# Kernel optimization log

Hardware: AMD Instinct MI355X
Metric: run time of the kernel (lower is better)

Reference implementation:

```python
import jax, jax.numpy as jnp
import numpy as np

B, P, D, VP, VD = 256, 1152, 10, 8, 16
NUM_ITER = 3


def setup_inputs() -> dict:
    key = jax.random.key(0)
    k1, k2 = jax.random.split(key)
    x = jax.random.normal(k1, (B, P, VP, 1), dtype=jnp.float32)
    # learned transform matrices, init randn/100 as in the torch module
    W = jax.random.normal(k2, (P, D, VD, VP), dtype=jnp.float32) / 100.0
    return {"x": x, "W": W}


def _squash(s, axis):
    # v = ||s||^2/(1+||s||^2) * s/||s||
    sq = jnp.sum(s * s, axis=axis, keepdims=True)
    return s * sq / (1.0 + sq) / jnp.sqrt(sq + 1e-9)


def reference(x, W):
    xs = x[..., 0]                                      # [B,P,8]
    # u_hat[b,p,d,:] = W[p,d] @ x[b,p]  (no explicit stack/broadcast materialization)
    u_hat = jnp.einsum('pdij,bpj->bpdi', W, xs)          # [B,P,D,16]
    u_stop = jax.lax.stop_gradient(u_hat)
    b_ij = jnp.zeros((B, P, D, 1), dtype=u_hat.dtype)    # torch b_ij [B,P,D,1,1], trailing 1 dropped
    v = None
    for it in range(NUM_ITER):
        # faithful to source: softmax over torch dim=3 (size-1 axis) -> all ones
        c_ij = jax.nn.softmax(b_ij, axis=3)               # [B,P,D,1]
        u = u_hat if it == NUM_ITER - 1 else u_stop
        s_j = jnp.sum(c_ij * u, axis=1)                   # [B,D,16]
        v = _squash(s_j, axis=2)                          # [B,D,16]
        if it != NUM_ITER - 1:
            # agreement: u_hat^T v -> scalar per (b,p,d)
            upd = jnp.einsum('bpdi,bdi->bpd', u_hat, v)[..., None]
            b_ij = b_ij + upd
    return v[..., None]                                   # [B,D,16,1] matching torch output
```

## Files before the change

### kernel.cpp

```cpp
#include <hip/hip_runtime.h>
#include <hip/hip_bf16.h>
#include <math.h>

#define M 256
#define N 160
#define K 9216
#define CH 32
#define KC 288
#define BM 32
#define XST 104

using f32x4 = __attribute__((ext_vector_type(4))) float;
using bf16x8 = __attribute__((ext_vector_type(8))) short;

__device__ __forceinline__ ushort f2bf(float f) {
  return __builtin_bit_cast(ushort, __float2bfloat16(f));
}

template <bool ATOMIC>
__global__ __launch_bounds__(256) void gemm_mfma(const float* __restrict__ x,
                                                 const float* __restrict__ W,
                                                 float* __restrict__ part) {
  __shared__ ushort Wl[12 * 1280];
  __shared__ ushort Xl[BM * XST];

  const int t = threadIdx.x;
  const int bx = blockIdx.x;
  const int mt = bx & 7;
  const int c = bx >> 3;
  const int m0 = mt * BM;
  const int k0 = c * KC;

  const int w = t >> 6;
  const int l = t & 63;
  const int lr = l & 15;
  const int lg = l >> 4;
  const int msub = w & 1;
  const int nh = w >> 1;

  float4 wv[15], xv[3];
  int xrow[3], xkq[3];
#pragma unroll
  for (int q = 0; q < 3; ++q) {
    const int f = t + 256 * q;
    xrow[q] = f / 24;
    xkq[q] = (f - xrow[q] * 24) * 4;
  }

  auto load = [&](int s) {
    const float* wsp = W + ((size_t)c * 36 + s * 12) * 1280;
#pragma unroll
    for (int q = 0; q < 15; ++q)
      wv[q] = *(const float4*)(wsp + 4 * (size_t)(t + 256 * q));
    const float* xs = x + (size_t)m0 * K + k0 + s * 96;
#pragma unroll
    for (int q = 0; q < 3; ++q)
      xv[q] = *(const float4*)(xs + (size_t)xrow[q] * K + xkq[q]);
  };
  auto put = [&]() {
#pragma unroll
    for (int q = 0; q < 15; ++q) {
      const int f4 = t + 256 * q;
      ushort4 h = {f2bf(wv[q].x), f2bf(wv[q].y), f2bf(wv[q].z), f2bf(wv[q].w)};
      *(ushort4*)&Wl[4 * f4] = h;
    }
#pragma unroll
    for (int q = 0; q < 3; ++q) {
      ushort4 h = {f2bf(xv[q].x), f2bf(xv[q].y), f2bf(xv[q].z), f2bf(xv[q].w)};
      *(ushort4*)&Xl[xrow[q] * XST + xkq[q]] = h;
    }
  };

  f32x4 acc[5];
#pragma unroll
  for (int nt = 0; nt < 5; ++nt) acc[nt] = {0.f, 0.f, 0.f, 0.f};

  auto comp = [&]() {
#pragma unroll
    for (int ks = 0; ks < 3; ++ks) {
      const bf16x8 a =
          *(const bf16x8*)&Xl[(msub * 16 + lr) * XST + ks * 32 + lg * 8];
#pragma unroll
      for (int nt = 0; nt < 5; ++nt) {
        const bf16x8 b =
            *(const bf16x8*)&Wl[(ks * 4 + lg) * 1280 + (nh * 5 + nt) * 128 +
                                lr * 8];
        acc[nt] =
            __builtin_amdgcn_mfma_f32_16x16x32_bf16(a, b, acc[nt], 0, 0, 0);
      }
    }
  };

  load(0);
  put();
  __syncthreads();
  load(1);
  comp();
  __syncthreads();
  put();
  __syncthreads();
  load(2);
  comp();
  __syncthreads();
  put();
  __syncthreads();
  comp();

  if (ATOMIC) {
#pragma unroll
    for (int nt = 0; nt < 5; ++nt)
#pragma unroll
      for (int r = 0; r < 4; ++r) {
        const int row = m0 + msub * 16 + lg * 4 + r;
        atomicAdd(&part[(size_t)row * N + (nh * 5 + nt) * 16 + lr],
                  acc[nt][r]);
      }
  } else {
    float* dst = part + (size_t)c * (M * N);
#pragma unroll
    for (int nt = 0; nt < 5; ++nt)
#pragma unroll
      for (int r = 0; r < 4; ++r) {
        const int row = m0 + msub * 16 + lg * 4 + r;
        dst[(size_t)row * N + (nh * 5 + nt) * 16 + lr] = acc[nt][r];
      }
  }
}

__global__ __launch_bounds__(256) void reduce_squash4(
    const float* __restrict__ part, float* __restrict__ out) {
  __shared__ f32x4 red[256];
  const int t = threadIdx.x;
  const int o4 = t & 63;
  const int slice = t >> 6;
  const f32x4* p4 = (const f32x4*)part;
  const int base4 = blockIdx.x * 64;

  f32x4 sum = {0.f, 0.f, 0.f, 0.f};
#pragma unroll
  for (int cc = 0; cc < 8; ++cc) {
    const int c = slice * 8 + cc;
    sum += p4[(size_t)c * (M * N / 4) + base4 + o4];
  }
  red[t] = sum;
  __syncthreads();
  if (t < 64) {
    const f32x4 s = red[t] + red[t + 64] + red[t + 128] + red[t + 192];
    float n2 = s[0] * s[0] + s[1] * s[1] + s[2] * s[2] + s[3] * s[3];
    n2 += __shfl_xor(n2, 1);
    n2 += __shfl_xor(n2, 2);
    const float sc = n2 / (1.0f + n2) / sqrtf(n2 + 1e-9f);
    f32x4 o = {s[0] * sc, s[1] * sc, s[2] * sc, s[3] * sc};
    ((f32x4*)out)[base4 + t] = o;
  }
}

__global__ __launch_bounds__(256) void squash_k(float* __restrict__ out) {
  const int e = blockIdx.x * 256 + threadIdx.x;
  const float s = out[e];
  float s2 = s * s;
  s2 += __shfl_xor(s2, 1);
  s2 += __shfl_xor(s2, 2);
  s2 += __shfl_xor(s2, 4);
  s2 += __shfl_xor(s2, 8);
  out[e] = s * s2 / (1.0f + s2) / sqrtf(s2 + 1e-9f);
}

extern "C" void kernel_launch(void* const* d_in, const int* in_sizes, int n_in,
                              void* d_out, int out_size, void* d_ws,
                              size_t ws_size, hipStream_t stream) {
  const float* x = (const float*)d_in[0];
  const float* W = (const float*)d_in[1];
  float* out = (float*)d_out;

  const size_t need = (size_t)CH * M * N * sizeof(float);
  if (ws_size >= need) {
    gemm_mfma<false><<<256, 256, 0, stream>>>(x, W, (float*)d_ws);
    reduce_squash4<<<(M * N) / 256, 256, 0, stream>>>((const float*)d_ws, out);
  } else {
    hipMemsetAsync(out, 0, (size_t)M * N * sizeof(float), stream);
    gemm_mfma<true><<<256, 256, 0, stream>>>(x, W, out);
    squash_k<<<(M * N) / 256, 256, 0, stream>>>(out);
  }
}
```

Baseline: 18.43 us.

## Fuse split-K reduction and squash into GEMM via per-tile arrival counters

Replaces the separate reduce_squash kernel with a tail inside the GEMM kernel. Each of the 256 blocks writes its partial tile, then increments a per-M-tile atomic counter. The last four blocks to arrive spin until all 32 chunks are done, and each reduces and squashes an 8-row slice. This removes one kernel launch and its dependency gap, at the cost of a memset launch for the counters, spin-waiting, and a reduction spread over only 32 blocks.

```diff
diff --git a/kernel.cpp b/kernel.cpp
--- a/kernel.cpp
+++ b/kernel.cpp
@@ -10,6 +10,8 @@
 #define BM 32
 #define XST 104
 
+#define PART_F32 ((size_t)CH * M * N)
+
 using f32x4 = __attribute__((ext_vector_type(4))) float;
 using bf16x8 = __attribute__((ext_vector_type(8))) short;
 
@@ -17,12 +19,14 @@
   return __builtin_bit_cast(ushort, __float2bfloat16(f));
 }
 
-template <bool ATOMIC>
-__global__ __launch_bounds__(256) void gemm_mfma(const float* __restrict__ x,
-                                                 const float* __restrict__ W,
-                                                 float* __restrict__ part) {
+__global__ __launch_bounds__(256) void fused_gemm(const float* __restrict__ x,
+                                                  const float* __restrict__ W,
+                                                  float* __restrict__ part,
+                                                  int* __restrict__ cnt,
+                                                  float* __restrict__ out) {
   __shared__ ushort Wl[12 * 1280];
-  __shared__ ushort Xl[BM * XST];
+  __shared__ __align__(16) ushort Xl[BM * XST];
+  __shared__ int s_old;
 
   const int t = threadIdx.x;
   const int bx = blockIdx.x;
@@ -106,16 +110,7 @@
   __syncthreads();
   comp();
 
-  if (ATOMIC) {
-#pragma unroll
-    for (int nt = 0; nt < 5; ++nt)
-#pragma unroll
-      for (int r = 0; r < 4; ++r) {
-        const int row = m0 + msub * 16 + lg * 4 + r;
-        atomicAdd(&part[(size_t)row * N + (nh * 5 + nt) * 16 + lr],
-                  acc[nt][r]);
-      }
-  } else {
+  {
     float* dst = part + (size_t)c * (M * N);
 #pragma unroll
     for (int nt = 0; nt < 5; ++nt)
@@ -125,34 +120,158 @@
         dst[(size_t)row * N + (nh * 5 + nt) * 16 + lr] = acc[nt][r];
       }
   }
-}
-
-__global__ __launch_bounds__(256) void reduce_squash4(
-    const float* __restrict__ part, float* __restrict__ out) {
-  __shared__ f32x4 red[256];
+
+  __threadfence();
+  __syncthreads();
+  if (t == 0)
+    s_old = __hip_atomic_fetch_add(&cnt[mt], 1, __ATOMIC_ACQ_REL,
+                                   __HIP_MEMORY_SCOPE_AGENT);
+  __syncthreads();
+  const int old = s_old;
+  if (old < CH - 4) return;
+  const int q = old - (CH - 4);
+
+  if (t == 0) {
+    while (__hip_atomic_load(&cnt[mt], __ATOMIC_ACQUIRE,
+                             __HIP_MEMORY_SCOPE_AGENT) < CH) {
+    }
+  }
+  __syncthreads();
+  __threadfence();
+
+  f32x4* sm = (f32x4*)Xl;
+  const f32x4* p4 = (const f32x4*)part;
+  const int rbase = m0 + q * 8;
+  {
+    const int v = t;
+    const int row_l = v / 40;
+    const int n4 = v - row_l * 40;
+    const int vi = (rbase + row_l) * 40 + n4;
+    f32x4 s = {0.f, 0.f, 0.f, 0.f};
+#pragma unroll 8
+    for (int cc = 0; cc < CH; ++cc) s += p4[(size_t)cc * (M * N / 4) + vi];
+    sm[v] = s;
+  }
+  if (t < 64) {
+    const int v = 256 + t;
+    const int row_l = v / 40;
+    const int n4 = v - row_l * 40;
+    const int vi = (rbase + row_l) * 40 + n4;
+    f32x4 s = {0.f, 0.f, 0.f, 0.f};
+#pragma unroll 8
+    for (int cc = 0; cc < CH; ++cc) s += p4[(size_t)cc * (M * N / 4) + vi];
+    sm[v] = s;
+  }
+  __syncthreads();
+
+  if (t < 80) {
+    const int row_l = t / 10;
+    const int cb4 = (t - row_l * 10) * 4;
+    const f32x4 a = sm[row_l * 40 + cb4 + 0];
+    const f32x4 b = sm[row_l * 40 + cb4 + 1];
+    const f32x4 cq = sm[row_l * 40 + cb4 + 2];
+    const f32x4 d = sm[row_l * 40 + cb4 + 3];
+    float n2 = a[0] * a[0] + a[1] * a[1] + a[2] * a[2] + a[3] * a[3] +
+               b[0] * b[0] + b[1] * b[1] + b[2] * b[2] + b[3] * b[3] +
+               cq[0] * cq[0] + cq[1] * cq[1] + cq[2] * cq[2] + cq[3] * cq[3] +
+               d[0] * d[0] + d[1] * d[1] + d[2] * d[2] + d[3] * d[3];
+    const float sc = n2 / (1.0f + n2) / sqrtf(n2 + 1e-9f);
+    f32x4* o4 = (f32x4*)out;
+    const int ob = (rbase + row_l) * 40 + cb4;
+    o4[ob + 0] = a * sc;
+    o4[ob + 1] = b * sc;
+    o4[ob + 2] = cq * sc;
+    o4[ob + 3] = d * sc;
+  }
+}
+
+__global__ __launch_bounds__(256) void gemm_atomic(const float* __restrict__ x,
+                                                   const float* __restrict__ W,
+                                                   float* __restrict__ outp) {
+  __shared__ ushort Wl[12 * 1280];
+  __shared__ ushort Xl[BM * XST];
   const int t = threadIdx.x;
-  const int o4 = t & 63;
-  const int slice = t >> 6;
-  const f32x4* p4 = (const f32x4*)part;
-  const int base4 = blockIdx.x * 64;
-
-  f32x4 sum = {0.f, 0.f, 0.f, 0.f};
-#pragma unroll
-  for (int cc = 0; cc < 8; ++cc) {
-    const int c = slice * 8 + cc;
-    sum += p4[(size_t)c * (M * N / 4) + base4 + o4];
-  }
-  red[t] = sum;
-  __syncthreads();
-  if (t < 64) {
-    const f32x4 s = red[t] + red[t + 64] + red[t + 128] + red[t + 192];
-    float n2 = s[0] * s[0] + s[1] * s[1] + s[2] * s[2] + s[3] * s[3];
-    n2 += __shfl_xor(n2, 1);
-    n2 += __shfl_xor(n2, 2);
-    const float sc = n2 / (1.0f + n2) / sqrtf(n2 + 1e-9f);
-    f32x4 o = {s[0] * sc, s[1] * sc, s[2] * sc, s[3] * sc};
-    ((f32x4*)out)[base4 + t] = o;
-  }
+  const int bx = blockIdx.x;
+  const int mt = bx & 7;
+  const int c = bx >> 3;
+  const int m0 = mt * BM;
+  const int k0 = c * KC;
+  const int w = t >> 6;
+  const int l = t & 63;
+  const int lr = l & 15;
+  const int lg = l >> 4;
+  const int msub = w & 1;
+  const int nh = w >> 1;
+  float4 wv[15], xv[3];
+  int xrow[3], xkq[3];
+#pragma unroll
+  for (int q = 0; q < 3; ++q) {
+    const int f = t + 256 * q;
+    xrow[q] = f / 24;
+    xkq[q] = (f - xrow[q] * 24) * 4;
+  }
+  auto load = [&](int s) {
+    const float* wsp = W + ((size_t)c * 36 + s * 12) * 1280;
+#pragma unroll
+    for (int q = 0; q < 15; ++q)
+      wv[q] = *(const float4*)(wsp + 4 * (size_t)(t + 256 * q));
+    const float* xs = x + (size_t)m0 * K + k0 + s * 96;
+#pragma unroll
+    for (int q = 0; q < 3; ++q)
+      xv[q] = *(const float4*)(xs + (size_t)xrow[q] * K + xkq[q]);
+  };
+  auto put = [&]() {
+#pragma unroll
+    for (int q = 0; q < 15; ++q) {
+      const int f4 = t + 256 * q;
+      ushort4 h = {f2bf(wv[q].x), f2bf(wv[q].y), f2bf(wv[q].z), f2bf(wv[q].w)};
+      *(ushort4*)&Wl[4 * f4] = h;
+    }
+#pragma unroll
+    for (int q = 0; q < 3; ++q) {
+      ushort4 h = {f2bf(xv[q].x), f2bf(xv[q].y), f2bf(xv[q].z), f2bf(xv[q].w)};
+      *(ushort4*)&Xl[xrow[q] * XST + xkq[q]] = h;
+    }
+  };
+  f32x4 acc[5];
+#pragma unroll
+  for (int nt = 0; nt < 5; ++nt) acc[nt] = {0.f, 0.f, 0.f, 0.f};
+  auto comp = [&]() {
+#pragma unroll
+    for (int ks = 0; ks < 3; ++ks) {
+      const bf16x8 a =
+          *(const bf16x8*)&Xl[(msub * 16 + lr) * XST + ks * 32 + lg * 8];
+#pragma unroll
+      for (int nt = 0; nt < 5; ++nt) {
+        const bf16x8 b =
+            *(const bf16x8*)&Wl[(ks * 4 + lg) * 1280 + (nh * 5 + nt) * 128 +
+                                lr * 8];
+        acc[nt] =
+            __builtin_amdgcn_mfma_f32_16x16x32_bf16(a, b, acc[nt], 0, 0, 0);
+      }
+    }
+  };
+  load(0);
+  put();
+  __syncthreads();
+  load(1);
+  comp();
+  __syncthreads();
+  put();
+  __syncthreads();
+  load(2);
+  comp();
+  __syncthreads();
+  put();
+  __syncthreads();
+  comp();
+#pragma unroll
+  for (int nt = 0; nt < 5; ++nt)
+#pragma unroll
+    for (int r = 0; r < 4; ++r) {
+      const int row = m0 + msub * 16 + lg * 4 + r;
+      atomicAdd(&outp[(size_t)row * N + (nh * 5 + nt) * 16 + lr], acc[nt][r]);
+    }
 }
 
 __global__ __launch_bounds__(256) void squash_k(float* __restrict__ out) {
@@ -173,13 +292,15 @@
   const float* W = (const float*)d_in[1];
   float* out = (float*)d_out;
 
-  const size_t need = (size_t)CH * M * N * sizeof(float);
+  const size_t need = PART_F32 * sizeof(float) + 64;
   if (ws_size >= need) {
-    gemm_mfma<false><<<256, 256, 0, stream>>>(x, W, (float*)d_ws);
-    reduce_squash4<<<(M * N) / 256, 256, 0, stream>>>((const float*)d_ws, out);
+    float* part = (float*)d_ws;
+    int* cnt = (int*)((char*)d_ws + PART_F32 * sizeof(float));
+    hipMemsetAsync(cnt, 0, 8 * sizeof(int), stream);
+    fused_gemm<<<256, 256, 0, stream>>>(x, W, part, cnt, out);
   } else {
     hipMemsetAsync(out, 0, (size_t)M * N * sizeof(float), stream);
-    gemm_mfma<true><<<256, 256, 0, stream>>>(x, W, out);
+    gemm_atomic<<<256, 256, 0, stream>>>(x, W, out);
     squash_k<<<(M * N) / 256, 256, 0, stream>>>(out);
   }
 }
```

Measured after the change: 55.95 us. 204% more time.

## Split K into 72 chunks with double-buffered padded W tiles

Applied to the files above, without the earlier changes.

Splits K into 72 chunks of 128 instead of 32 chunks of 288, which raises the GEMM grid from 256 to 576 blocks. X is now loaded once up front. W is streamed in four stages through a double-buffered, padded LDS layout so the next stage's global loads overlap the MFMA work. The trade-off is more partial sums written to the workspace and a larger reduction, now 18 chunks per slice, in the squash kernel.

```diff
diff --git a/kernel.cpp b/kernel.cpp
--- a/kernel.cpp
+++ b/kernel.cpp
@@ -5,10 +5,11 @@
 #define M 256
 #define N 160
 #define K 9216
-#define CH 32
-#define KC 288
+#define CH 72
+#define KC 128
 #define BM 32
-#define XST 104
+#define WPS 1296
+#define XSTR 136
 
 using f32x4 = __attribute__((ext_vector_type(4))) float;
 using bf16x8 = __attribute__((ext_vector_type(8))) short;
@@ -21,8 +22,8 @@
 __global__ __launch_bounds__(256) void gemm_mfma(const float* __restrict__ x,
                                                  const float* __restrict__ W,
                                                  float* __restrict__ part) {
-  __shared__ ushort Wl[12 * 1280];
-  __shared__ ushort Xl[BM * XST];
+  __shared__ __align__(16) ushort Wl[2][4 * WPS];
+  __shared__ __align__(16) ushort Xl[BM * XSTR];
 
   const int t = threadIdx.x;
   const int bx = blockIdx.x;
@@ -38,36 +39,34 @@
   const int msub = w & 1;
   const int nh = w >> 1;
 
-  float4 wv[15], xv[3];
-  int xrow[3], xkq[3];
+  {
+    const float* xs = x + (size_t)m0 * K + k0;
 #pragma unroll
-  for (int q = 0; q < 3; ++q) {
-    const int f = t + 256 * q;
-    xrow[q] = f / 24;
-    xkq[q] = (f - xrow[q] * 24) * 4;
+    for (int q = 0; q < 4; ++q) {
+      const int f = t + 256 * q;
+      const int row = f >> 5;
+      const int kq4 = f & 31;
+      const float4 v = *(const float4*)(xs + (size_t)row * K + kq4 * 4);
+      ushort4 h = {f2bf(v.x), f2bf(v.y), f2bf(v.z), f2bf(v.w)};
+      *(ushort4*)&Xl[row * XSTR + kq4 * 4] = h;
+    }
   }
 
-  auto load = [&](int s) {
-    const float* wsp = W + ((size_t)c * 36 + s * 12) * 1280;
+  float4 wv[5];
+  auto loadW = [&](int s) {
+    const float* wsp = W + ((size_t)c * 16 + s * 4) * 1280;
 #pragma unroll
-    for (int q = 0; q < 15; ++q)
+    for (int q = 0; q < 5; ++q)
       wv[q] = *(const float4*)(wsp + 4 * (size_t)(t + 256 * q));
-    const float* xs = x + (size_t)m0 * K + k0 + s * 96;
+  };
+  auto putW = [&](int b) {
 #pragma unroll
-    for (int q = 0; q < 3; ++q)
-      xv[q] = *(const float4*)(xs + (size_t)xrow[q] * K + xkq[q]);
-  };
-  auto put = [&]() {
-#pragma unroll
-    for (int q = 0; q < 15; ++q) {
-      const int f4 = t + 256 * q;
+    for (int q = 0; q < 5; ++q) {
+      const int e = t + 256 * q;
+      const int pl = e / 320;
+      const int r4 = e - pl * 320;
       ushort4 h = {f2bf(wv[q].x), f2bf(wv[q].y), f2bf(wv[q].z), f2bf(wv[q].w)};
-      *(ushort4*)&Wl[4 * f4] = h;
-    }
-#pragma unroll
-    for (int q = 0; q < 3; ++q) {
-      ushort4 h = {f2bf(xv[q].x), f2bf(xv[q].y), f2bf(xv[q].z), f2bf(xv[q].w)};
-      *(ushort4*)&Xl[xrow[q] * XST + xkq[q]] = h;
+      *(ushort4*)&Wl[b][pl * WPS + r4 * 4] = h;
     }
   };
 
@@ -75,36 +74,33 @@
 #pragma unroll
   for (int nt = 0; nt < 5; ++nt) acc[nt] = {0.f, 0.f, 0.f, 0.f};
 
-  auto comp = [&]() {
+  auto comp = [&](int b, int s) {
+    const bf16x8 a =
+        *(const bf16x8*)&Xl[(msub * 16 + lr) * XSTR + s * 32 + lg * 8];
 #pragma unroll
-    for (int ks = 0; ks < 3; ++ks) {
-      const bf16x8 a =
-          *(const bf16x8*)&Xl[(msub * 16 + lr) * XST + ks * 32 + lg * 8];
-#pragma unroll
-      for (int nt = 0; nt < 5; ++nt) {
-        const bf16x8 b =
-            *(const bf16x8*)&Wl[(ks * 4 + lg) * 1280 + (nh * 5 + nt) * 128 +
-                                lr * 8];
-        acc[nt] =
-            __builtin_amdgcn_mfma_f32_16x16x32_bf16(a, b, acc[nt], 0, 0, 0);
-      }
+    for (int nt = 0; nt < 5; ++nt) {
+      const bf16x8 bb =
+          *(const bf16x8*)&Wl[b][lg * WPS + (nh * 5 + nt) * 128 + lr * 8];
+      acc[nt] = __builtin_amdgcn_mfma_f32_16x16x32_bf16(a, bb, acc[nt], 0, 0, 0);
     }
   };
 
-  load(0);
-  put();
+  loadW(0);
+  putW(0);
   __syncthreads();
-  load(1);
-  comp();
+  loadW(1);
+  comp(0, 0);
+  putW(1);
   __syncthreads();
-  put();
+  loadW(2);
+  comp(1, 1);
+  putW(0);
   __syncthreads();
-  load(2);
-  comp();
+  loadW(3);
+  comp(0, 2);
+  putW(1);
   __syncthreads();
-  put();
-  __syncthreads();
-  comp();
+  comp(1, 3);
 
   if (ATOMIC) {
 #pragma unroll
@@ -137,9 +133,9 @@
   const int base4 = blockIdx.x * 64;
 
   f32x4 sum = {0.f, 0.f, 0.f, 0.f};
-#pragma unroll
-  for (int cc = 0; cc < 8; ++cc) {
-    const int c = slice * 8 + cc;
+#pragma unroll 6
+  for (int cc = 0; cc < 18; ++cc) {
+    const int c = slice * 18 + cc;
     sum += p4[(size_t)c * (M * N / 4) + base4 + o4];
   }
   red[t] = sum;
@@ -175,11 +171,11 @@
 
   const size_t need = (size_t)CH * M * N * sizeof(float);
   if (ws_size >= need) {
-    gemm_mfma<false><<<256, 256, 0, stream>>>(x, W, (float*)d_ws);
+    gemm_mfma<false><<<8 * CH, 256, 0, stream>>>(x, W, (float*)d_ws);
     reduce_squash4<<<(M * N) / 256, 256, 0, stream>>>((const float*)d_ws, out);
   } else {
     hipMemsetAsync(out, 0, (size_t)M * N * sizeof(float), stream);
-    gemm_mfma<true><<<256, 256, 0, stream>>>(x, W, out);
+    gemm_mfma<true><<<8 * CH, 256, 0, stream>>>(x, W, out);
     squash_k<<<(M * N) / 256, 256, 0, stream>>>(out);
   }
 }
```

Result: slower. 20.73 us (+12.5%).
